# Kernel tuning notes

Measured on AMD Instinct MI355X. Metric: run time of the kernel, lower is better.

The kernel has to match this reference:

```python
import jax, jax.numpy as jnp
import numpy as np

B, S, D, E, K = 64, 1024, 1024, 8, 2
Z_COEF = 1e-3      # router_z_loss_coef
AUX_COEF = 1e-3    # router_aux_loss_coef


def setup_inputs() -> dict:
    key = jax.random.key(0)
    k1, k2, k3 = jax.random.split(key, 3)
    x = jax.random.normal(k1, (B, S, D), dtype=jnp.float32)
    # xavier-uniform-ish init for query weight, randn for expert keys (as in torch init)
    lim_q = float(np.sqrt(6.0 / (D + D)))
    Wq = jax.random.uniform(k2, (D, D), dtype=jnp.float32, minval=-lim_q, maxval=lim_q)
    bq = jnp.zeros((D,), dtype=jnp.float32)
    lim_k = float(np.sqrt(6.0 / (E + D)))
    key_emb = jax.random.uniform(k3, (E, D), dtype=jnp.float32, minval=-lim_k, maxval=lim_k)
    return {"x": x, "Wq": Wq, "bq": bq, "key_emb": key_emb}


def reference(x, Wq, bq, key_emb):
    b, s, d = x.shape
    e = key_emb.shape[0]
    scale = d ** (-0.5)

    # q = Linear(x); attn over expert keys
    q = jnp.einsum('bsd,od->bso', x, Wq) + bq              # [B,S,D]
    attn_scores = jnp.einsum('bsd,ed->bse', q, key_emb) * scale  # [B,S,E]
    attn_weights = jax.nn.softmax(attn_scores, axis=-1)    # [B,S,E]

    # per-batch expert scores, top-k selection, scatter mask
    scores = attn_weights.mean(axis=1)                     # [B,E]
    top_k_scores, top_k_indices = jax.lax.top_k(scores, K)  # [B,K]
    mask2d = jnp.zeros_like(scores).at[jnp.arange(b)[:, None], top_k_indices].set(1.0)  # [B,E]
    mask = jnp.broadcast_to(mask2d[:, None, :], (b, s, e))  # [B,S,E]

    # routing loss: KL(load-balance) + entropy-style aux
    total_tokens = b * s
    expert_usage_prob = mask2d.sum(axis=0) * (s / total_tokens)   # == mask.sum((0,1))/total
    ideal_prob = jnp.full((e,), 1.0 / e, dtype=scores.dtype)
    # F.kl_div(log_input, target, reduction='batchmean'): sum(t*(log t - log_in))/batch(=E)
    kl = jnp.sum(ideal_prob * (jnp.log(ideal_prob) - jnp.log(expert_usage_prob))) / e
    aux = jnp.mean(attn_weights * jnp.log(attn_weights + 1e-9))
    router_loss = Z_COEF * kl + AUX_COEF * aux

    return mask, top_k_indices, router_loss
```

## Files before the change

kernel.cpp:

```cpp
#include <hip/hip_runtime.h>
#include <math.h>

#define W2OFF  0
#define B2OFF  8192
#define SCOFF  8200
#define AUXOFF 8712
#define ZTOT   513

__global__ __launch_bounds__(256) void k01_prep(const float* __restrict__ Wq,
                                                const float* __restrict__ key,
                                                const float* __restrict__ bq,
                                                float* __restrict__ ws) {
    __shared__ __attribute__((aligned(16))) float keyl[8 * 1024];
    __shared__ float part[256 * 8];
    int tid = threadIdx.x;
    int blk = blockIdx.x;

    if (blk == 0) {
        #pragma unroll
        for (int k = 0; k < 3; ++k) {
            int i = tid + 256 * k;
            if (i < ZTOT) ws[SCOFF + i] = 0.0f;
        }
    }

    float4* kl4 = (float4*)keyl;
    const float4* kg4 = (const float4*)key;
    #pragma unroll
    for (int k = 0; k < 8; ++k) kl4[tid + 256 * k] = kg4[tid + 256 * k];
    __syncthreads();

    int dl = tid & 15;
    int og = tid >> 4;
    int d  = blk * 16 + dl;
    float acc[8];
    #pragma unroll
    for (int e = 0; e < 8; ++e) acc[e] = 0.0f;
    for (int oo = 0; oo < 64; ++oo) {
        int o = og * 64 + oo;
        float wv = Wq[o * 1024 + d];
        #pragma unroll
        for (int e = 0; e < 8; ++e) acc[e] += keyl[e * 1024 + o] * wv;
    }
    #pragma unroll
    for (int e = 0; e < 8; ++e) part[tid * 8 + e] = acc[e];
    __syncthreads();
    if (tid < 128) {
        int dl2 = tid >> 3, e = tid & 7;
        float s = 0.0f;
        #pragma unroll
        for (int g = 0; g < 16; ++g) s += part[(g * 16 + dl2) * 8 + e];
        ws[W2OFF + e * 1024 + blk * 16 + dl2] = s;
    }

    if (blk == 0) {
        __syncthreads();
        float p[8];
        #pragma unroll
        for (int e = 0; e < 8; ++e) p[e] = 0.0f;
        #pragma unroll
        for (int k = 0; k < 4; ++k) {
            int d2 = tid + 256 * k;
            float bv = bq[d2];
            #pragma unroll
            for (int e = 0; e < 8; ++e) p[e] += bv * keyl[e * 1024 + d2];
        }
        #pragma unroll
        for (int e = 0; e < 8; ++e) part[tid * 8 + e] = p[e];
        __syncthreads();
        if (tid < 8) {
            float s = 0.0f;
            for (int k = 0; k < 256; ++k) s += part[k * 8 + tid];
            ws[B2OFF + tid] = s;
        }
    }
}

__global__ __launch_bounds__(256) void k2_main(const float* __restrict__ x,
                                               float* __restrict__ ws) {
    __shared__ __attribute__((aligned(16))) float w2l[8 * 1024];
    __shared__ __attribute__((aligned(16))) float part[4 * 64 * 8];

    int tid  = threadIdx.x;
    int blk  = blockIdx.x;
    int lane = tid & 63;
    int w    = tid >> 6;
    int batch = blk >> 4;
    int tb    = blk * 64;
    int e = lane & 7;
    int r = lane >> 3;

    float4* wl4 = (float4*)w2l;
    const float4* wg4 = (const float4*)(ws + W2OFF);
    #pragma unroll
    for (int k = 0; k < 8; ++k) wl4[tid + 256 * k] = wg4[tid + 256 * k];
    float b2v = ws[B2OFF + e];
    __syncthreads();

    const float4* x4 = (const float4*)x;
    float* pw = part + w * 512;
    const float scale = 0.03125f;
    float sc_acc = 0.0f, aux_acc = 0.0f;

    for (int p = 0; p < 4; ++p) {
        int lt0 = w * 16 + p * 4;
        int t0  = tb + lt0;
        float acc[4][8];
        #pragma unroll
        for (int j = 0; j < 4; ++j)
            #pragma unroll
            for (int c = 0; c < 8; ++c) acc[j][c] = 0.0f;

        #pragma unroll
        for (int i = 0; i < 4; ++i) {
            float4 xr[4];
            #pragma unroll
            for (int j = 0; j < 4; ++j)
                xr[j] = x4[(size_t)(t0 + j) * 256 + i * 64 + lane];
            #pragma unroll
            for (int c = 0; c < 8; ++c) {
                float4 w4 = wl4[c * 256 + i * 64 + lane];
                #pragma unroll
                for (int j = 0; j < 4; ++j)
                    acc[j][c] += w4.x * xr[j].x + w4.y * xr[j].y +
                                 w4.z * xr[j].z + w4.w * xr[j].w;
            }
        }

        #pragma unroll
        for (int j = 0; j < 4; ++j) {
            #pragma unroll
            for (int c = 0; c < 8; ++c)
                pw[c * 64 + (lane ^ (c << 3))] = acc[j][c];
            float s = 0.0f;
            #pragma unroll
            for (int m = 0; m < 8; ++m)
                s += pw[e * 64 + ((r + 8 * m) ^ (e << 3))];
            s += __shfl_xor(s, 8);
            s += __shfl_xor(s, 16);
            s += __shfl_xor(s, 32);
            float sv = (s + b2v) * scale;
            float mx = sv;
            mx = fmaxf(mx, __shfl_xor(mx, 1));
            mx = fmaxf(mx, __shfl_xor(mx, 2));
            mx = fmaxf(mx, __shfl_xor(mx, 4));
            float ex = expf(sv - mx);
            float sm = ex;
            sm += __shfl_xor(sm, 1);
            sm += __shfl_xor(sm, 2);
            sm += __shfl_xor(sm, 4);
            float wgt = ex / sm;
            sc_acc  += wgt;
            aux_acc += wgt * logf(wgt + 1e-9f);
        }
    }

    if (r == 0) atomicAdd(&ws[SCOFF + batch * 8 + e], sc_acc);
    #pragma unroll
    for (int mk = 1; mk <= 32; mk <<= 1) aux_acc += __shfl_xor(aux_acc, mk);
    if (lane == 0) atomicAdd(&ws[AUXOFF], aux_acc * 0.125f);
}

__device__ __forceinline__ void top2_of8(const float* v, int& i1, int& i2) {
    i1 = 0; float b1 = v[0];
    #pragma unroll
    for (int e = 1; e < 8; ++e) if (v[e] > b1) { b1 = v[e]; i1 = e; }
    i2 = -1; float b2 = -3.4e38f;
    #pragma unroll
    for (int e = 0; e < 8; ++e) if (e != i1 && v[e] > b2) { b2 = v[e]; i2 = e; }
}

__global__ __launch_bounds__(256) void k3_out(const float* __restrict__ ws,
                                              float* __restrict__ out) {
    int tid = threadIdx.x;
    int blk = blockIdx.x;
    int batch = blk >> 2;

    float v[8];
    #pragma unroll
    for (int e = 0; e < 8; ++e) v[e] = ws[SCOFF + batch * 8 + e];
    int i1, i2;
    top2_of8(v, i1, i2);

    float m[8];
    #pragma unroll
    for (int e = 0; e < 8; ++e) m[e] = (e == i1 || e == i2) ? 1.0f : 0.0f;
    int token = blk * 256 + tid;
    float4* o4 = (float4*)out;
    o4[token * 2]     = make_float4(m[0], m[1], m[2], m[3]);
    o4[token * 2 + 1] = make_float4(m[4], m[5], m[6], m[7]);

    if (blk == 0) {
        __shared__ int cnt[8];
        if (tid < 8) cnt[tid] = 0;
        __syncthreads();
        if (tid < 64) {
            float vv[8];
            #pragma unroll
            for (int e = 0; e < 8; ++e) vv[e] = ws[SCOFF + tid * 8 + e];
            int j1, j2;
            top2_of8(vv, j1, j2);
            out[524288 + tid * 2]     = (float)j1;
            out[524288 + tid * 2 + 1] = (float)j2;
            atomicAdd(&cnt[j1], 1);
            atomicAdd(&cnt[j2], 1);
        }
        __syncthreads();
        if (tid == 0) {
            float kl = 0.0f;
            #pragma unroll
            for (int e = 0; e < 8; ++e) {
                float usage = (float)cnt[e] / 64.0f;
                kl += 0.125f * (logf(0.125f) - logf(usage));
            }
            kl *= 0.125f;
            float aux = ws[AUXOFF] / 524288.0f;
            out[524416] = 1e-3f * kl + 1e-3f * aux;
        }
    }
}

extern "C" void kernel_launch(void* const* d_in, const int* in_sizes, int n_in,
                              void* d_out, int out_size, void* d_ws, size_t ws_size,
                              hipStream_t stream) {
    const float* x   = (const float*)d_in[0];
    const float* Wq  = (const float*)d_in[1];
    const float* bq  = (const float*)d_in[2];
    const float* key = (const float*)d_in[3];
    float* out = (float*)d_out;
    float* ws  = (float*)d_ws;

    k01_prep<<<64,   256, 0, stream>>>(Wq, key, bq, ws);
    k2_main<<<1024, 256, 0, stream>>>(x, ws);
    k3_out <<<256,  256, 0, stream>>>(ws, out);
}
```

Baseline: 410.1 us.

## Defer softmax to one wave per block and reduce partial sums by expert

Each wave now reduces its per-token dot-product partials grouped by expert, with lanes arranged expert-major, and writes raw scores to shared memory. A single wave then computes softmax, entropy and per-expert sums for the block's 64 tokens, replacing the shuffle-heavy per-token softmax that every wave ran. The change also spreads zeroing of the score workspace across all prep blocks and makes the bias-key dot reduction two-stage. This cuts redundant exp/log work and shuffles, but adds a block barrier and leaves the tail serialized on one wave while the other waves sit idle.

```diff
diff --git a/kernel.cpp b/kernel.cpp
--- a/kernel.cpp
+++ b/kernel.cpp
@@ -13,15 +13,13 @@
                                                 float* __restrict__ ws) {
     __shared__ __attribute__((aligned(16))) float keyl[8 * 1024];
     __shared__ float part[256 * 8];
+    __shared__ float part2[64];
     int tid = threadIdx.x;
     int blk = blockIdx.x;
 
-    if (blk == 0) {
-        #pragma unroll
-        for (int k = 0; k < 3; ++k) {
-            int i = tid + 256 * k;
-            if (i < ZTOT) ws[SCOFF + i] = 0.0f;
-        }
+    if (tid < 9) {
+        int i = blk * 9 + tid;
+        if (i < ZTOT) ws[SCOFF + i] = 0.0f;
     }
 
     float4* kl4 = (float4*)keyl;
@@ -68,9 +66,18 @@
         #pragma unroll
         for (int e = 0; e < 8; ++e) part[tid * 8 + e] = p[e];
         __syncthreads();
+        if (tid < 64) {
+            int e = tid & 7, g = tid >> 3;
+            float s = 0.0f;
+            #pragma unroll
+            for (int k = 0; k < 32; ++k) s += part[(g * 32 + k) * 8 + e];
+            part2[g * 8 + e] = s;
+        }
+        __syncthreads();
         if (tid < 8) {
             float s = 0.0f;
-            for (int k = 0; k < 256; ++k) s += part[k * 8 + tid];
+            #pragma unroll
+            for (int g = 0; g < 8; ++g) s += part2[g * 8 + tid];
             ws[B2OFF + tid] = s;
         }
     }
@@ -80,6 +87,7 @@
                                                float* __restrict__ ws) {
     __shared__ __attribute__((aligned(16))) float w2l[8 * 1024];
     __shared__ __attribute__((aligned(16))) float part[4 * 64 * 8];
+    __shared__ __attribute__((aligned(16))) float sraw[64 * 8];
 
     int tid  = threadIdx.x;
     int blk  = blockIdx.x;
@@ -87,20 +95,17 @@
     int w    = tid >> 6;
     int batch = blk >> 4;
     int tb    = blk * 64;
-    int e = lane & 7;
-    int r = lane >> 3;
+    int e = lane >> 3;
+    int r = lane & 7;
 
     float4* wl4 = (float4*)w2l;
     const float4* wg4 = (const float4*)(ws + W2OFF);
     #pragma unroll
     for (int k = 0; k < 8; ++k) wl4[tid + 256 * k] = wg4[tid + 256 * k];
-    float b2v = ws[B2OFF + e];
     __syncthreads();
 
     const float4* x4 = (const float4*)x;
     float* pw = part + w * 512;
-    const float scale = 0.03125f;
-    float sc_acc = 0.0f, aux_acc = 0.0f;
 
     for (int p = 0; p < 4; ++p) {
         int lt0 = w * 16 + p * 4;
@@ -136,29 +141,54 @@
             #pragma unroll
             for (int m = 0; m < 8; ++m)
                 s += pw[e * 64 + ((r + 8 * m) ^ (e << 3))];
-            s += __shfl_xor(s, 8);
-            s += __shfl_xor(s, 16);
-            s += __shfl_xor(s, 32);
-            float sv = (s + b2v) * scale;
-            float mx = sv;
-            mx = fmaxf(mx, __shfl_xor(mx, 1));
-            mx = fmaxf(mx, __shfl_xor(mx, 2));
-            mx = fmaxf(mx, __shfl_xor(mx, 4));
-            float ex = expf(sv - mx);
-            float sm = ex;
-            sm += __shfl_xor(sm, 1);
-            sm += __shfl_xor(sm, 2);
-            sm += __shfl_xor(sm, 4);
-            float wgt = ex / sm;
-            sc_acc  += wgt;
-            aux_acc += wgt * logf(wgt + 1e-9f);
-        }
-    }
-
-    if (r == 0) atomicAdd(&ws[SCOFF + batch * 8 + e], sc_acc);
-    #pragma unroll
-    for (int mk = 1; mk <= 32; mk <<= 1) aux_acc += __shfl_xor(aux_acc, mk);
-    if (lane == 0) atomicAdd(&ws[AUXOFF], aux_acc * 0.125f);
+            s += __shfl_xor(s, 1);
+            s += __shfl_xor(s, 2);
+            s += __shfl_xor(s, 4);
+            if (r == 0) sraw[(lt0 + j) * 8 + e] = s;
+        }
+    }
+    __syncthreads();
+
+    if (tid < 64) {
+        int t = tid;
+        float sv[8];
+        #pragma unroll
+        for (int k = 0; k < 8; ++k) {
+            int c = (t + k) & 7;
+            sv[c] = sraw[t * 8 + c];
+        }
+        const float scale = 0.03125f;
+        #pragma unroll
+        for (int c = 0; c < 8; ++c) sv[c] = (sv[c] + ws[B2OFF + c]) * scale;
+        float mx = sv[0];
+        #pragma unroll
+        for (int c = 1; c < 8; ++c) mx = fmaxf(mx, sv[c]);
+        float wgt[8], sm = 0.0f;
+        #pragma unroll
+        for (int c = 0; c < 8; ++c) { wgt[c] = expf(sv[c] - mx); sm += wgt[c]; }
+        float inv = 1.0f / sm;
+        float aux = 0.0f;
+        #pragma unroll
+        for (int c = 0; c < 8; ++c) {
+            wgt[c] *= inv;
+            aux += wgt[c] * logf(wgt[c] + 1e-9f);
+        }
+        #pragma unroll
+        for (int c = 0; c < 8; ++c)
+            part[c * 64 + (t ^ (c << 3))] = wgt[c];
+        int e2 = t >> 3, r2 = t & 7;
+        float s2 = 0.0f;
+        #pragma unroll
+        for (int m = 0; m < 8; ++m)
+            s2 += part[e2 * 64 + ((r2 + 8 * m) ^ (e2 << 3))];
+        s2 += __shfl_xor(s2, 1);
+        s2 += __shfl_xor(s2, 2);
+        s2 += __shfl_xor(s2, 4);
+        if (r2 == 0) atomicAdd(&ws[SCOFF + batch * 8 + e2], s2);
+        #pragma unroll
+        for (int mk = 1; mk <= 32; mk <<= 1) aux += __shfl_xor(aux, mk);
+        if (t == 0) atomicAdd(&ws[AUXOFF], aux);
+    }
 }
 
 __device__ __forceinline__ void top2_of8(const float* v, int& i1, int& i2) {
```

After: 384.1 us. 1.07x faster.
